# Performance work log

Hardware: AMD Instinct MI355X
Metric: run time of the kernel (lower is better)

The kernel has to match this reference:

```python
import jax, jax.numpy as jnp
import numpy as np

S, O, H = 8, 1024, 1024
B, N = 32, 512

def setup_inputs() -> dict:
    key = jax.random.key(0)
    k1, k2, k3, k4 = jax.random.split(key, 4)
    x = jax.random.normal(k1, (B, N, H), dtype=jnp.float32)
    subject_id = jax.random.randint(k2, (B,), 0, S)
    # kaiming_uniform_(a=sqrt(5)) on [S,O,H]: fan_in=H, gain=sqrt(2/(1+5)), bound=gain*sqrt(3/fan_in)
    wbound = jnp.sqrt(2.0 / 6.0) * jnp.sqrt(3.0 / H)
    weight = jax.random.uniform(k3, (S, O, H), minval=-wbound, maxval=wbound, dtype=jnp.float32)
    bbound = 1.0 / jnp.sqrt(H)
    bias = jax.random.uniform(k4, (S, O), minval=-bbound, maxval=bbound, dtype=jnp.float32)
    return {"x": x, "subject_id": subject_id, "weight": weight, "bias": bias}

def reference(x, subject_id, weight, bias):
    # Per-sample weight gather + batched matmul + bias add
    W = weight[subject_id]          # [B, O, H]
    b = bias[subject_id]            # [B, O]
    y = jnp.einsum('bnh,boh->bno', x, W) + b[:, None, :]
    return y
```

## Files before the change

### kernel.cpp

```cpp
#include <hip/hip_runtime.h>


constexpr int S_DIM = 8;
constexpr int O_DIM = 1024;
constexpr int H_DIM = 1024;
constexpr int B_DIM = 32;
constexpr int N_DIM = 512;

constexpr int BM = 128;
constexpr int BN = 128;
constexpr int BK = 64;
constexpr int LDK = BK + 8;
constexpr int NTHREADS = 256;

typedef short bf16x8 __attribute__((ext_vector_type(8)));
typedef float f32x4 __attribute__((ext_vector_type(4)));
typedef float f32x2 __attribute__((ext_vector_type(2)));
typedef __bf16 bf16x2 __attribute__((ext_vector_type(2)));

__device__ __forceinline__ unsigned int cvt_pk_bf16(float a, float b) {
  f32x2 v;
  v[0] = a;
  v[1] = b;
  bf16x2 r = __builtin_convertvector(v, bf16x2);
  return __builtin_bit_cast(unsigned int, r);
}

__global__ __launch_bounds__(NTHREADS, 1) void scl_gemm(
    const float* __restrict__ x, const int* __restrict__ subject_id,
    const float* __restrict__ weight, const float* __restrict__ bias,
    float* __restrict__ out) {
  __shared__ __align__(16) unsigned short As[BM * LDK];
  __shared__ __align__(16) unsigned short Bs[BN * LDK];

  const int tid = threadIdx.x;
  const int b = blockIdx.z;
  const int n0 = blockIdx.x * BM;
  const int o0 = blockIdx.y * BN;
  const int sid = subject_id[b];

  const int lane = tid & 63;
  const int wid = tid >> 6;
  const int wm0 = (wid >> 1) * 64;
  const int wn0 = (wid & 1) * 64;
  const int lcol = lane & 15;
  const int lq = lane >> 4;

  const int srow = tid >> 4;
  const int sc4 = (tid & 15) * 4;

  const float* xp = x + (size_t)(b * N_DIM + n0 + srow) * H_DIM + sc4;
  const float* wp = weight + (size_t)(sid * O_DIM + o0 + srow) * H_DIM + sc4;

  f32x4 acc[4][4];
#pragma unroll
  for (int mi = 0; mi < 4; ++mi)
#pragma unroll
    for (int ni = 0; ni < 4; ++ni) {
      f32x4 z = {0.f, 0.f, 0.f, 0.f};
      acc[mi][ni] = z;
    }

  for (int k0 = 0; k0 < H_DIM; k0 += BK) {
    __syncthreads();
#pragma unroll
    for (int i = 0; i < 8; ++i) {
      const int r = srow + i * 16;
      const f32x4 va = *(const f32x4*)(xp + (size_t)(i * 16) * H_DIM + k0);
      const f32x4 vb = *(const f32x4*)(wp + (size_t)(i * 16) * H_DIM + k0);
      uint2 ua, ub;
      ua.x = cvt_pk_bf16(va[0], va[1]);
      ua.y = cvt_pk_bf16(va[2], va[3]);
      ub.x = cvt_pk_bf16(vb[0], vb[1]);
      ub.y = cvt_pk_bf16(vb[2], vb[3]);
      *(uint2*)(&As[r * LDK + sc4]) = ua;
      *(uint2*)(&Bs[r * LDK + sc4]) = ub;
    }
    __syncthreads();

#pragma unroll
    for (int kk = 0; kk < BK; kk += 32) {
      const int kb = kk + lq * 8;
      bf16x8 af[4], bfr[4];
#pragma unroll
      for (int mi = 0; mi < 4; ++mi)
        af[mi] = *(const bf16x8*)(&As[(wm0 + mi * 16 + lcol) * LDK + kb]);
#pragma unroll
      for (int ni = 0; ni < 4; ++ni)
        bfr[ni] = *(const bf16x8*)(&Bs[(wn0 + ni * 16 + lcol) * LDK + kb]);
#pragma unroll
      for (int mi = 0; mi < 4; ++mi)
#pragma unroll
        for (int ni = 0; ni < 4; ++ni)
          acc[mi][ni] = __builtin_amdgcn_mfma_f32_16x16x32_bf16(
              af[mi], bfr[ni], acc[mi][ni], 0, 0, 0);
    }
  }

  float bv[4];
#pragma unroll
  for (int ni = 0; ni < 4; ++ni)
    bv[ni] = bias[sid * O_DIM + o0 + wn0 + ni * 16 + lcol];

  float* outb = out + (size_t)(b * N_DIM + n0 + wm0) * O_DIM + o0 + wn0 + lcol;
#pragma unroll
  for (int mi = 0; mi < 4; ++mi) {
#pragma unroll
    for (int r = 0; r < 4; ++r) {
      float* orow = outb + (size_t)(mi * 16 + lq * 4 + r) * O_DIM;
#pragma unroll
      for (int ni = 0; ni < 4; ++ni)
        orow[ni * 16] = acc[mi][ni][r] + bv[ni];
    }
  }
}

extern "C" void kernel_launch(void* const* d_in, const int* in_sizes, int n_in,
                              void* d_out, int out_size, void* d_ws, size_t ws_size,
                              hipStream_t stream) {
  const float* x = (const float*)d_in[0];
  const int* subject_id = (const int*)d_in[1];
  const float* weight = (const float*)d_in[2];
  const float* bias = (const float*)d_in[3];
  float* out = (float*)d_out;

  dim3 grid(N_DIM / BM, O_DIM / BN, B_DIM);
  scl_gemm<<<grid, NTHREADS, 0, stream>>>(x, subject_id, weight, bias, out);
}
```

Measured before the change: 208.5 us.

## Pre-convert inputs to bf16 and stage tiles via direct global-to-LDS loads

Adds a separate conversion pass that writes bf16 copies of x and all weights into workspace. The GEMM then loads bf16 tiles straight into LDS with global_load_lds instead of loading fp32 into registers, converting and storing. It also drops the LDS row padding and raises the occupancy hint in launch bounds. In exchange it adds an extra full read of x and W plus a bf16 write, and the unpadded LDS layout may cause bank conflicts on the fragment reads.

```diff
diff --git a/kernel.cpp b/kernel.cpp
--- a/kernel.cpp
+++ b/kernel.cpp
@@ -10,8 +10,11 @@
 constexpr int BM = 128;
 constexpr int BN = 128;
 constexpr int BK = 64;
-constexpr int LDK = BK + 8;
 constexpr int NTHREADS = 256;
+
+constexpr long long X_ELEMS = (long long)B_DIM * N_DIM * H_DIM;
+constexpr long long W_ELEMS = (long long)S_DIM * O_DIM * H_DIM;
+constexpr size_t XB_BYTES = (size_t)X_ELEMS * 2;
 
 typedef short bf16x8 __attribute__((ext_vector_type(8)));
 typedef float f32x4 __attribute__((ext_vector_type(4)));
@@ -26,12 +29,42 @@
   return __builtin_bit_cast(unsigned int, r);
 }
 
-__global__ __launch_bounds__(NTHREADS, 1) void scl_gemm(
-    const float* __restrict__ x, const int* __restrict__ subject_id,
-    const float* __restrict__ weight, const float* __restrict__ bias,
+__device__ __forceinline__ void gload_lds16(const void* g, void* l) {
+  __builtin_amdgcn_global_load_lds(
+      (const __attribute__((address_space(1))) unsigned int*)g,
+      (__attribute__((address_space(3))) unsigned int*)l, 16, 0, 0);
+}
+
+__global__ __launch_bounds__(256) void cvt_kernel(
+    const float* __restrict__ x, const float* __restrict__ w,
+    unsigned short* __restrict__ xb, unsigned short* __restrict__ wb) {
+  const long long t = (long long)blockIdx.x * 256 + threadIdx.x;
+  const long long XT = X_ELEMS / 8;
+  const float* src;
+  unsigned short* dst;
+  long long i;
+  if (t < XT) {
+    src = x; dst = xb; i = t;
+  } else {
+    src = w; dst = wb; i = t - XT;
+  }
+  const f32x4* p = (const f32x4*)(src + i * 8);
+  const f32x4 a = p[0];
+  const f32x4 c = p[1];
+  uint4 u;
+  u.x = cvt_pk_bf16(a[0], a[1]);
+  u.y = cvt_pk_bf16(a[2], a[3]);
+  u.z = cvt_pk_bf16(c[0], c[1]);
+  u.w = cvt_pk_bf16(c[2], c[3]);
+  *(uint4*)(dst + i * 8) = u;
+}
+
+__global__ __launch_bounds__(NTHREADS, 4) void scl_gemm(
+    const unsigned short* __restrict__ xb, const int* __restrict__ subject_id,
+    const unsigned short* __restrict__ wb, const float* __restrict__ bias,
     float* __restrict__ out) {
-  __shared__ __align__(16) unsigned short As[BM * LDK];
-  __shared__ __align__(16) unsigned short Bs[BN * LDK];
+  __shared__ __align__(16) unsigned short As[BM * BK];
+  __shared__ __align__(16) unsigned short Bs[BN * BK];
 
   const int tid = threadIdx.x;
   const int b = blockIdx.z;
@@ -46,11 +79,12 @@
   const int lcol = lane & 15;
   const int lq = lane >> 4;
 
-  const int srow = tid >> 4;
-  const int sc4 = (tid & 15) * 4;
-
-  const float* xp = x + (size_t)(b * N_DIM + n0 + srow) * H_DIM + sc4;
-  const float* wp = weight + (size_t)(sid * O_DIM + o0 + srow) * H_DIM + sc4;
+  const int srow = wid * 32 + (lane >> 3);
+  const int skc = (lane & 7) * 8;
+  const unsigned short* ag = xb + (size_t)(b * N_DIM + n0 + srow) * H_DIM + skc;
+  const unsigned short* bg = wb + (size_t)(sid * O_DIM + o0 + srow) * H_DIM + skc;
+  unsigned short* as_base = &As[(wid * 32) * BK];
+  unsigned short* bs_base = &Bs[(wid * 32) * BK];
 
   f32x4 acc[4][4];
 #pragma unroll
@@ -64,17 +98,9 @@
   for (int k0 = 0; k0 < H_DIM; k0 += BK) {
     __syncthreads();
 #pragma unroll
-    for (int i = 0; i < 8; ++i) {
-      const int r = srow + i * 16;
-      const f32x4 va = *(const f32x4*)(xp + (size_t)(i * 16) * H_DIM + k0);
-      const f32x4 vb = *(const f32x4*)(wp + (size_t)(i * 16) * H_DIM + k0);
-      uint2 ua, ub;
-      ua.x = cvt_pk_bf16(va[0], va[1]);
-      ua.y = cvt_pk_bf16(va[2], va[3]);
-      ub.x = cvt_pk_bf16(vb[0], vb[1]);
-      ub.y = cvt_pk_bf16(vb[2], vb[3]);
-      *(uint2*)(&As[r * LDK + sc4]) = ua;
-      *(uint2*)(&Bs[r * LDK + sc4]) = ub;
+    for (int i = 0; i < 4; ++i) {
+      gload_lds16(ag + (size_t)(i * 8) * H_DIM + k0, as_base + i * 8 * BK);
+      gload_lds16(bg + (size_t)(i * 8) * H_DIM + k0, bs_base + i * 8 * BK);
     }
     __syncthreads();
 
@@ -84,10 +110,10 @@
       bf16x8 af[4], bfr[4];
 #pragma unroll
       for (int mi = 0; mi < 4; ++mi)
-        af[mi] = *(const bf16x8*)(&As[(wm0 + mi * 16 + lcol) * LDK + kb]);
+        af[mi] = *(const bf16x8*)(&As[(wm0 + mi * 16 + lcol) * BK + kb]);
 #pragma unroll
       for (int ni = 0; ni < 4; ++ni)
-        bfr[ni] = *(const bf16x8*)(&Bs[(wn0 + ni * 16 + lcol) * LDK + kb]);
+        bfr[ni] = *(const bf16x8*)(&Bs[(wn0 + ni * 16 + lcol) * BK + kb]);
 #pragma unroll
       for (int mi = 0; mi < 4; ++mi)
 #pragma unroll
@@ -124,6 +150,12 @@
   const float* bias = (const float*)d_in[3];
   float* out = (float*)d_out;
 
+  unsigned short* xb = (unsigned short*)d_ws;
+  unsigned short* wb = (unsigned short*)((char*)d_ws + XB_BYTES);
+
+  const long long cvt_threads = (X_ELEMS + W_ELEMS) / 8;
+  cvt_kernel<<<(int)(cvt_threads / 256), 256, 0, stream>>>(x, weight, xb, wb);
+
   dim3 grid(N_DIM / BM, O_DIM / BN, B_DIM);
-  scl_gemm<<<grid, NTHREADS, 0, stream>>>(x, subject_id, weight, bias, out);
+  scl_gemm<<<grid, NTHREADS, 0, stream>>>(xb, subject_id, wb, bias, out);
 }
```

Result: faster. 188.8 us (-9.5%).
